# Kernel optimization log

Hardware: AMD Instinct MI355X
Metric: run time of the kernel (lower is better)

The kernel has to match this reference:

```python
import jax, jax.numpy as jnp
import numpy as np

NUM_EMBEDDINGS = 768
HEAD_SIZE = 64

def setup_inputs() -> dict:
    key = jax.random.key(0)
    kx, kq, kk, kv = jax.random.split(key, 4)
    B, T, E, H = 4, 2048, NUM_EMBEDDINGS, HEAD_SIZE
    x = jax.random.normal(kx, (B, T, E), dtype=jnp.float32)
    s = 1.0 / np.sqrt(E)
    Wq = jax.random.normal(kq, (E, H), dtype=jnp.float32) * s
    Wk = jax.random.normal(kk, (E, H), dtype=jnp.float32) * s
    Wv = jax.random.normal(kv, (E, H), dtype=jnp.float32) * s
    return {"x": x, "Wq": Wq, "Wk": Wk, "Wv": Wv}

def reference(x, Wq, Wk, Wv):
    # x: [B,T,E]; Wq/Wk/Wv: [E,H]
    q = x @ Wq  # [B,T,H]
    k = x @ Wk
    v = x @ Wv
    scores = jnp.einsum('bth,bsh->bts', q, k) * (k.shape[-1] ** -0.5)  # [B,T,T]
    T = scores.shape[-1]
    # torch.tril(ones, diagonal=-1).bool(): True strictly below diagonal (t > s)
    row = jnp.arange(T)[:, None]
    col = jnp.arange(T)[None, :]
    mask = row > col  # strictly lower triangle masked to -inf
    scores = jnp.where(mask, -jnp.inf, scores)
    attn = jax.nn.softmax(scores, axis=-1)
    return attn @ v  # [B,T,H]
```

## Files before the change

### kernel.cpp

```cpp
#include <hip/hip_runtime.h>
#include <hip/hip_bf16.h>

#define T_ 2048
#define E_ 768

typedef __attribute__((ext_vector_type(8))) __bf16 bf16x8;
typedef __attribute__((ext_vector_type(8))) unsigned short ushort8;
typedef __attribute__((ext_vector_type(4))) unsigned short ushort4v;
typedef __attribute__((ext_vector_type(4))) float floatx4;

static __device__ __forceinline__ unsigned short f2bf(float f) {
    union { float f; unsigned u; } v; v.f = f;
    unsigned u = v.u;
    u += 0x7FFFu + ((u >> 16) & 1u);
    return (unsigned short)(u >> 16);
}

static __device__ __forceinline__ float bf2f(unsigned short s) {
    union { unsigned u; float f; } v; v.u = ((unsigned)s) << 16;
    return v.f;
}

__global__ __launch_bounds__(256) void prep_wT(const float* __restrict__ Wq,
                                               const float* __restrict__ Wk,
                                               const float* __restrict__ Wv,
                                               unsigned short* __restrict__ wT) {
    int w  = blockIdx.x / 12;
    int k0 = (blockIdx.x % 12) * 64;
    const float* W = (w == 0) ? Wq : (w == 1 ? Wk : Wv);
    __shared__ unsigned short sm[64][65];
    int tid = threadIdx.x;
    #pragma unroll
    for (int i = 0; i < 16; ++i) {
        int idx = tid + i * 256;
        int k = idx >> 6, n = idx & 63;
        sm[n][k] = f2bf(W[(size_t)(k0 + k) * 64 + n]);
    }
    __syncthreads();
    #pragma unroll
    for (int i = 0; i < 16; ++i) {
        int idx = tid + i * 256;
        int n = idx >> 6, k = idx & 63;
        wT[(size_t)w * (64 * 768) + (size_t)n * 768 + k0 + k] = sm[n][k];
    }
}

__global__ __launch_bounds__(256) void qkv_proj(const float* __restrict__ x,
                                                const unsigned short* __restrict__ wT,
                                                unsigned short* __restrict__ Qb,
                                                unsigned short* __restrict__ Kb,
                                                unsigned short* __restrict__ vT) {
    __shared__ unsigned short ws_[192][72];
    __shared__ unsigned short xs[16][72];

    int tid  = threadIdx.x;
    int lane = tid & 63, wv = tid >> 6;
    int lrow = lane & 15;
    int kh   = lane >> 4;
    int lk   = kh * 8;
    int t0   = blockIdx.x * 16;
    int n0   = wv * 48;

    int wr = tid >> 3;
    int wc = (tid & 7) * 8;
    int xr = tid >> 4;
    int xc = (tid & 15) * 4;

    floatx4 acc[3] = {};

    for (int k0 = 0; k0 < 768; k0 += 64) {
        #pragma unroll
        for (int c = 0; c < 6; ++c) {
            int rw = c * 32 + wr;
            *(ushort8*)&ws_[rw][wc] = *(const ushort8*)(wT + (size_t)rw * 768 + k0 + wc);
        }
        {
            float4 a = *(const float4*)(x + (size_t)(t0 + xr) * 768 + k0 + xc);
            ushort4v p;
            p[0] = f2bf(a.x); p[1] = f2bf(a.y); p[2] = f2bf(a.z); p[3] = f2bf(a.w);
            *(ushort4v*)&xs[xr][xc] = p;
        }
        __syncthreads();
        #pragma unroll
        for (int kc = 0; kc < 2; ++kc) {
            bf16x8 af = *(const bf16x8*)&xs[lrow][kc * 32 + lk];
            #pragma unroll
            for (int nf = 0; nf < 3; ++nf) {
                bf16x8 bfv = *(const bf16x8*)&ws_[n0 + nf * 16 + lrow][kc * 32 + lk];
                acc[nf] = __builtin_amdgcn_mfma_f32_16x16x32_bf16(af, bfv, acc[nf], 0, 0, 0);
            }
        }
        __syncthreads();
    }

    const float QS = 0.18033688011112042f;
    int mt = t0 + kh * 4;
    #pragma unroll
    for (int nf = 0; nf < 3; ++nf) {
        int nb   = n0 + nf * 16;
        int widx = nb >> 6;
        int col  = (nb & 63) + lrow;
        if (widx == 0) {
            #pragma unroll
            for (int rg = 0; rg < 4; ++rg)
                Qb[(size_t)(mt + rg) * 64 + col] = f2bf(acc[nf][rg] * QS);
        } else if (widx == 1) {
            #pragma unroll
            for (int rg = 0; rg < 4; ++rg)
                Kb[(size_t)(mt + rg) * 64 + col] = f2bf(acc[nf][rg]);
        } else {
            int b  = mt >> 11;
            int tl = mt & 2047;
            ushort4v pk;
            #pragma unroll
            for (int rg = 0; rg < 4; ++rg) pk[rg] = f2bf(acc[nf][rg]);
            *(ushort4v*)&vT[(size_t)(b * 64 + col) * T_ + tl] = pk;
        }
    }
}

__global__ __launch_bounds__(256) void attn_one(const unsigned short* __restrict__ Qb,
                                                const unsigned short* __restrict__ Kb,
                                                const unsigned short* __restrict__ vT,
                                                float* __restrict__ lP,
                                                unsigned short* __restrict__ oP) {
    int c  = blockIdx.x;
    int qt = blockIdx.y;
    int b  = blockIdx.z;
    int t0 = qt * 64;
    int s0 = t0 + c * 64;
    if (s0 >= T_) return;

    __shared__ unsigned short ks[64][72];
    __shared__ unsigned short vts[64][72];
    __shared__ unsigned short ps[4][16][72];

    int tid  = threadIdx.x;
    int lane = tid & 63, wv = tid >> 6;
    int lrow = lane & 15;
    int lk   = (lane >> 4) * 8;
    int qrow4 = (lane >> 4) * 4;
    int sr = tid >> 2, sc = tid & 3;

    const ushort8* kp = (const ushort8*)(Kb + (size_t)(b * T_ + s0 + sr) * 64 + sc * 16);
    ushort8 ka = kp[0], kb = kp[1];
    const ushort8* vp = (const ushort8*)(vT + (size_t)(b * 64 + sr) * T_ + s0 + sc * 16);
    ushort8 va = vp[0], vb = vp[1];
    bf16x8 qf[2];
    {
        const unsigned short* qp = Qb + (size_t)(b * T_ + t0 + wv * 16 + lrow) * 64 + lk;
        qf[0] = *(const bf16x8*)(qp);
        qf[1] = *(const bf16x8*)(qp + 32);
    }
    *(ushort8*)&ks[sr][sc * 16]      = ka;
    *(ushort8*)&ks[sr][sc * 16 + 8]  = kb;
    *(ushort8*)&vts[sr][sc * 16]     = va;
    *(ushort8*)&vts[sr][sc * 16 + 8] = vb;
    __syncthreads();

    floatx4 sf[4] = {};
    #pragma unroll
    for (int kc = 0; kc < 2; ++kc) {
        bf16x8 af = qf[kc];
        #pragma unroll
        for (int nf = 0; nf < 4; ++nf) {
            bf16x8 bfv = *(const bf16x8*)&ks[nf * 16 + lrow][kc * 32 + lk];
            sf[nf] = __builtin_amdgcn_mfma_f32_16x16x32_bf16(af, bfv, sf[nf], 0, 0, 0);
        }
    }

    if (c == 0) {
        #pragma unroll
        for (int nf = 0; nf < 4; ++nf)
            #pragma unroll
            for (int rg = 0; rg < 4; ++rg) {
                int sl = nf * 16 + lrow;
                int ql = wv * 16 + qrow4 + rg;
                if (sl < ql) sf[nf][rg] = -__builtin_inff();
            }
    }

    float l_[4] = {0.f, 0.f, 0.f, 0.f};
    #pragma unroll
    for (int nf = 0; nf < 4; ++nf)
        #pragma unroll
        for (int rg = 0; rg < 4; ++rg) {
            float p = exp2f(sf[nf][rg]);
            l_[rg] += p;
            ps[wv][qrow4 + rg][nf * 16 + lrow] = f2bf(p);
        }

    floatx4 of[4] = {};
    #pragma unroll
    for (int kc = 0; kc < 2; ++kc) {
        bf16x8 pa = *(const bf16x8*)&ps[wv][lrow][kc * 32 + lk];
        #pragma unroll
        for (int hf = 0; hf < 4; ++hf) {
            bf16x8 vbv = *(const bf16x8*)&vts[hf * 16 + lrow][kc * 32 + lk];
            of[hf] = __builtin_amdgcn_mfma_f32_16x16x32_bf16(pa, vbv, of[hf], 0, 0, 0);
        }
    }

    int p = ((b * 32 + qt) << 5) + c;
    #pragma unroll
    for (int rg = 0; rg < 4; ++rg) {
        float v = l_[rg];
        v += __shfl_xor(v, 1, 64);
        v += __shfl_xor(v, 2, 64);
        v += __shfl_xor(v, 4, 64);
        v += __shfl_xor(v, 8, 64);
        l_[rg] = v;
    }
    if (lrow == 0) {
        #pragma unroll
        for (int rg = 0; rg < 4; ++rg) {
            int row = wv * 16 + qrow4 + rg;
            lP[(size_t)p * 64 + row] = l_[rg];
        }
    }
    #pragma unroll
    for (int hf = 0; hf < 4; ++hf)
        #pragma unroll
        for (int rg = 0; rg < 4; ++rg) {
            int row = wv * 16 + qrow4 + rg;
            oP[((size_t)p * 64 + row) * 64 + hf * 16 + lrow] = f2bf(of[hf][rg]);
        }
}

__global__ __launch_bounds__(256) void combine(const float* __restrict__ lP,
                                               const unsigned short* __restrict__ oP,
                                               float* __restrict__ out) {
    int bq = blockIdx.x >> 2;
    int rq = blockIdx.x & 3;
    int qt = bq & 31;
    int b  = bq >> 5;
    int nch = 32 - qt;

    int tid = threadIdx.x;
    int r   = rq * 16 + (tid >> 4);
    int cb  = (tid & 15) * 4;

    float L = 0.f;
    float4 o = {0.f, 0.f, 0.f, 0.f};
    for (int cc = 0; cc < nch; ++cc) {
        size_t p = (size_t)((bq << 5) + cc);
        L += lP[p * 64 + r];
        ushort4v ov = *(const ushort4v*)&oP[(p * 64 + r) * 64 + cb];
        o.x += bf2f(ov[0]); o.y += bf2f(ov[1]); o.z += bf2f(ov[2]); o.w += bf2f(ov[3]);
    }
    float inv = 1.0f / L;
    float4 res = {o.x * inv, o.y * inv, o.z * inv, o.w * inv};
    *(float4*)&out[((size_t)(b * T_ + qt * 64 + r)) * 64 + cb] = res;
}

extern "C" void kernel_launch(void* const* d_in, const int* in_sizes, int n_in,
                              void* d_out, int out_size, void* d_ws, size_t ws_size,
                              hipStream_t stream) {
    const float* x  = (const float*)d_in[0];
    const float* Wq = (const float*)d_in[1];
    const float* Wk = (const float*)d_in[2];
    const float* Wv = (const float*)d_in[3];
    float* out = (float*)d_out;

    unsigned short* wT = (unsigned short*)d_ws;
    unsigned short* Qb = wT + 3 * 64 * 768;
    unsigned short* Kb = Qb + 8192 * 64;
    unsigned short* vT = Kb + 8192 * 64;
    float* lP = (float*)(vT + 4 * 64 * T_);
    unsigned short* oP = (unsigned short*)(lP + 128 * 32 * 64);

    prep_wT<<<36, 256, 0, stream>>>(Wq, Wk, Wv, wT);
    qkv_proj<<<512, 256, 0, stream>>>(x, wT, Qb, Kb, vT);
    attn_one<<<dim3(32, 32, 4), 256, 0, stream>>>(Qb, Kb, vT, lP, oP);
    combine<<<512, 256, 0, stream>>>(lP, oP, out);
}
```

Baseline: 48.65 us.

## Process four key tiles per attention block with direct-to-LDS swizzled loads

Each attention block now covers up to four 64-key tiles instead of one and accumulates l and O across them, so there are fewer partials for the combine pass to read and fewer blocks to launch. K, V^T and the weight tiles are stored pre-swizzled in global memory and copied straight into unpadded LDS with global_load_lds, with XOR-swizzled reads to avoid bank conflicts. The cost is less parallelism per block, serial work inside each block, and a layout coupling between the producer and consumer kernels.

New measurement: 41.84 us. 1.16x faster.

```diff
diff --git a/kernel.cpp b/kernel.cpp
--- a/kernel.cpp
+++ b/kernel.cpp
@@ -19,6 +19,12 @@
 static __device__ __forceinline__ float bf2f(unsigned short s) {
     union { unsigned u; float f; } v; v.u = ((unsigned)s) << 16;
     return v.f;
+}
+
+static __device__ __forceinline__ void gload16(const void* g, void* l) {
+    __builtin_amdgcn_global_load_lds(
+        (const __attribute__((address_space(1))) void*)g,
+        (__attribute__((address_space(3))) void*)l, 16, 0, 0);
 }
 
 __global__ __launch_bounds__(256) void prep_wT(const float* __restrict__ Wq,
@@ -41,7 +47,9 @@
     for (int i = 0; i < 16; ++i) {
         int idx = tid + i * 256;
         int n = idx >> 6, k = idx & 63;
-        wT[(size_t)w * (64 * 768) + (size_t)n * 768 + k0 + k] = sm[n][k];
+        int ng = w * 64 + n;
+        int swzk = ((((k >> 3) & 7) ^ (ng & 7)) << 3) | (k & 7);
+        wT[(size_t)w * (64 * 768) + (size_t)n * 768 + k0 + swzk] = sm[n][k];
     }
 }
 
@@ -50,7 +58,7 @@
                                                 unsigned short* __restrict__ Qb,
                                                 unsigned short* __restrict__ Kb,
                                                 unsigned short* __restrict__ vT) {
-    __shared__ unsigned short ws_[192][72];
+    __shared__ unsigned short ws_[192][64];
     __shared__ unsigned short xs[16][72];
 
     int tid  = threadIdx.x;
@@ -61,18 +69,20 @@
     int t0   = blockIdx.x * 16;
     int n0   = wv * 48;
 
-    int wr = tid >> 3;
-    int wc = (tid & 7) * 8;
     int xr = tid >> 4;
     int xc = (tid & 15) * 4;
 
+    int wrow_l = (lane >> 3);
+    int wslot  = lane & 7;
+
     floatx4 acc[3] = {};
 
     for (int k0 = 0; k0 < 768; k0 += 64) {
         #pragma unroll
         for (int c = 0; c < 6; ++c) {
-            int rw = c * 32 + wr;
-            *(ushort8*)&ws_[rw][wc] = *(const ushort8*)(wT + (size_t)rw * 768 + k0 + wc);
+            int rbase = wv * 48 + c * 8;
+            const unsigned short* src = wT + (size_t)(rbase + wrow_l) * 768 + k0 + wslot * 8;
+            gload16(src, &ws_[rbase][0]);
         }
         {
             float4 a = *(const float4*)(x + (size_t)(t0 + xr) * 768 + k0 + xc);
@@ -84,9 +94,10 @@
         #pragma unroll
         for (int kc = 0; kc < 2; ++kc) {
             bf16x8 af = *(const bf16x8*)&xs[lrow][kc * 32 + lk];
+            int sl = (kc * 4 + kh) ^ (lrow & 7);
             #pragma unroll
             for (int nf = 0; nf < 3; ++nf) {
-                bf16x8 bfv = *(const bf16x8*)&ws_[n0 + nf * 16 + lrow][kc * 32 + lk];
+                bf16x8 bfv = *(const bf16x8*)&ws_[n0 + nf * 16 + lrow][sl << 3];
                 acc[nf] = __builtin_amdgcn_mfma_f32_16x16x32_bf16(af, bfv, acc[nf], 0, 0, 0);
             }
         }
@@ -106,20 +117,26 @@
                 Qb[(size_t)(mt + rg) * 64 + col] = f2bf(acc[nf][rg] * QS);
         } else if (widx == 1) {
             #pragma unroll
-            for (int rg = 0; rg < 4; ++rg)
-                Kb[(size_t)(mt + rg) * 64 + col] = f2bf(acc[nf][rg]);
+            for (int rg = 0; rg < 4; ++rg) {
+                int krow = mt + rg;
+                int g    = col >> 3;
+                int c2   = (((g ^ (krow & 7)) << 3)) | (col & 7);
+                Kb[(size_t)krow * 64 + c2] = f2bf(acc[nf][rg]);
+            }
         } else {
             int b  = mt >> 11;
             int tl = mt & 2047;
+            int h  = col;
+            int tswz = (tl & ~63) | ((((tl >> 3) & 7) ^ (h & 7)) << 3) | (tl & 7);
             ushort4v pk;
             #pragma unroll
             for (int rg = 0; rg < 4; ++rg) pk[rg] = f2bf(acc[nf][rg]);
-            *(ushort4v*)&vT[(size_t)(b * 64 + col) * T_ + tl] = pk;
-        }
-    }
-}
-
-__global__ __launch_bounds__(256) void attn_one(const unsigned short* __restrict__ Qb,
+            *(ushort4v*)&vT[(size_t)(b * 64 + h) * T_ + tswz] = pk;
+        }
+    }
+}
+
+__global__ __launch_bounds__(256) void attn_sum(const unsigned short* __restrict__ Qb,
                                                 const unsigned short* __restrict__ Kb,
                                                 const unsigned short* __restrict__ vT,
                                                 float* __restrict__ lP,
@@ -128,80 +145,92 @@
     int qt = blockIdx.y;
     int b  = blockIdx.z;
     int t0 = qt * 64;
-    int s0 = t0 + c * 64;
-    if (s0 >= T_) return;
-
-    __shared__ unsigned short ks[64][72];
-    __shared__ unsigned short vts[64][72];
+    int sBeg = t0 + c * 256;
+    if (sBeg >= T_) return;
+    int nt = (T_ - sBeg) >> 6; if (nt > 4) nt = 4;
+
+    __shared__ unsigned short ks4[4][64][64];
+    __shared__ unsigned short vts4[4][64][64];
     __shared__ unsigned short ps[4][16][72];
 
     int tid  = threadIdx.x;
     int lane = tid & 63, wv = tid >> 6;
     int lrow = lane & 15;
-    int lk   = (lane >> 4) * 8;
-    int qrow4 = (lane >> 4) * 4;
-    int sr = tid >> 2, sc = tid & 3;
-
-    const ushort8* kp = (const ushort8*)(Kb + (size_t)(b * T_ + s0 + sr) * 64 + sc * 16);
-    ushort8 ka = kp[0], kb = kp[1];
-    const ushort8* vp = (const ushort8*)(vT + (size_t)(b * 64 + sr) * T_ + s0 + sc * 16);
-    ushort8 va = vp[0], vb = vp[1];
+    int kh   = lane >> 4;
+    int lk   = kh * 8;
+    int qrow4 = kh * 4;
+    int rsub = lane >> 3;
+    int gsub = lane & 7;
+
+    for (int i = 0; i < nt; ++i) {
+        int s0 = sBeg + i * 64;
+        const unsigned short* ksrc = Kb + (size_t)(b * T_ + s0 + wv * 16 + rsub) * 64 + gsub * 8;
+        gload16(ksrc,                 &ks4[i][wv * 16][0]);
+        gload16(ksrc + 8 * 64,        &ks4[i][wv * 16 + 8][0]);
+        const unsigned short* vsrc = vT + (size_t)(b * 64 + wv * 16 + rsub) * T_ + s0 + gsub * 8;
+        gload16(vsrc,                 &vts4[i][wv * 16][0]);
+        gload16(vsrc + 8 * (size_t)T_, &vts4[i][wv * 16 + 8][0]);
+    }
+
     bf16x8 qf[2];
     {
         const unsigned short* qp = Qb + (size_t)(b * T_ + t0 + wv * 16 + lrow) * 64 + lk;
         qf[0] = *(const bf16x8*)(qp);
         qf[1] = *(const bf16x8*)(qp + 32);
     }
-    *(ushort8*)&ks[sr][sc * 16]      = ka;
-    *(ushort8*)&ks[sr][sc * 16 + 8]  = kb;
-    *(ushort8*)&vts[sr][sc * 16]     = va;
-    *(ushort8*)&vts[sr][sc * 16 + 8] = vb;
+
     __syncthreads();
 
-    floatx4 sf[4] = {};
-    #pragma unroll
-    for (int kc = 0; kc < 2; ++kc) {
-        bf16x8 af = qf[kc];
-        #pragma unroll
-        for (int nf = 0; nf < 4; ++nf) {
-            bf16x8 bfv = *(const bf16x8*)&ks[nf * 16 + lrow][kc * 32 + lk];
-            sf[nf] = __builtin_amdgcn_mfma_f32_16x16x32_bf16(af, bfv, sf[nf], 0, 0, 0);
-        }
-    }
-
-    if (c == 0) {
+    float l_[4] = {0.f, 0.f, 0.f, 0.f};
+    floatx4 of[4] = {};
+
+    for (int i = 0; i < nt; ++i) {
+        bool domask = (c == 0) && (i == 0);
+        floatx4 sf[4] = {};
+        #pragma unroll
+        for (int kc = 0; kc < 2; ++kc) {
+            bf16x8 af = qf[kc];
+            int sl = (kc * 4 + kh) ^ (lrow & 7);
+            #pragma unroll
+            for (int nf = 0; nf < 4; ++nf) {
+                bf16x8 bfv = *(const bf16x8*)&ks4[i][nf * 16 + lrow][sl << 3];
+                sf[nf] = __builtin_amdgcn_mfma_f32_16x16x32_bf16(af, bfv, sf[nf], 0, 0, 0);
+            }
+        }
+
+        if (domask) {
+            #pragma unroll
+            for (int nf = 0; nf < 4; ++nf)
+                #pragma unroll
+                for (int rg = 0; rg < 4; ++rg) {
+                    int slane = nf * 16 + lrow;
+                    int qlane = wv * 16 + qrow4 + rg;
+                    if (slane < qlane) sf[nf][rg] = -__builtin_inff();
+                }
+        }
+
         #pragma unroll
         for (int nf = 0; nf < 4; ++nf)
             #pragma unroll
             for (int rg = 0; rg < 4; ++rg) {
-                int sl = nf * 16 + lrow;
-                int ql = wv * 16 + qrow4 + rg;
-                if (sl < ql) sf[nf][rg] = -__builtin_inff();
-            }
-    }
-
-    float l_[4] = {0.f, 0.f, 0.f, 0.f};
-    #pragma unroll
-    for (int nf = 0; nf < 4; ++nf)
-        #pragma unroll
-        for (int rg = 0; rg < 4; ++rg) {
-            float p = exp2f(sf[nf][rg]);
-            l_[rg] += p;
-            ps[wv][qrow4 + rg][nf * 16 + lrow] = f2bf(p);
-        }
-
-    floatx4 of[4] = {};
-    #pragma unroll
-    for (int kc = 0; kc < 2; ++kc) {
-        bf16x8 pa = *(const bf16x8*)&ps[wv][lrow][kc * 32 + lk];
-        #pragma unroll
-        for (int hf = 0; hf < 4; ++hf) {
-            bf16x8 vbv = *(const bf16x8*)&vts[hf * 16 + lrow][kc * 32 + lk];
-            of[hf] = __builtin_amdgcn_mfma_f32_16x16x32_bf16(pa, vbv, of[hf], 0, 0, 0);
-        }
-    }
-
-    int p = ((b * 32 + qt) << 5) + c;
+                float p = exp2f(sf[nf][rg]);
+                l_[rg] += p;
+                ps[wv][qrow4 + rg][nf * 16 + lrow] = f2bf(p);
+            }
+
+        #pragma unroll
+        for (int kc = 0; kc < 2; ++kc) {
+            bf16x8 pa = *(const bf16x8*)&ps[wv][lrow][kc * 32 + lk];
+            int sl = (kc * 4 + kh) ^ (lrow & 7);
+            #pragma unroll
+            for (int hf = 0; hf < 4; ++hf) {
+                bf16x8 vbv = *(const bf16x8*)&vts4[i][hf * 16 + lrow][sl << 3];
+                of[hf] = __builtin_amdgcn_mfma_f32_16x16x32_bf16(pa, vbv, of[hf], 0, 0, 0);
+            }
+        }
+    }
+
+    int p = (b * 32 + qt) * 8 + c;
     #pragma unroll
     for (int rg = 0; rg < 4; ++rg) {
         float v = l_[rg];
@@ -234,7 +263,7 @@
     int rq = blockIdx.x & 3;
     int qt = bq & 31;
     int b  = bq >> 5;
-    int nch = 32 - qt;
+    int nch = (2303 - 64 * qt) >> 8;
 
     int tid = threadIdx.x;
     int r   = rq * 16 + (tid >> 4);
@@ -243,7 +272,7 @@
     float L = 0.f;
     float4 o = {0.f, 0.f, 0.f, 0.f};
     for (int cc = 0; cc < nch; ++cc) {
-        size_t p = (size_t)((bq << 5) + cc);
+        size_t p = (size_t)(bq * 8 + cc);
         L += lP[p * 64 + r];
         ushort4v ov = *(const ushort4v*)&oP[(p * 64 + r) * 64 + cb];
         o.x += bf2f(ov[0]); o.y += bf2f(ov[1]); o.z += bf2f(ov[2]); o.w += bf2f(ov[3]);
@@ -267,10 +296,10 @@
     unsigned short* Kb = Qb + 8192 * 64;
     unsigned short* vT = Kb + 8192 * 64;
     float* lP = (float*)(vT + 4 * 64 * T_);
-    unsigned short* oP = (unsigned short*)(lP + 128 * 32 * 64);
+    unsigned short* oP = (unsigned short*)(lP + 128 * 8 * 64);
 
     prep_wT<<<36, 256, 0, stream>>>(Wq, Wk, Wv, wT);
     qkv_proj<<<512, 256, 0, stream>>>(x, wT, Qb, Kb, vT);
-    attn_one<<<dim3(32, 32, 4), 256, 0, stream>>>(Qb, Kb, vT, lP, oP);
+    attn_sum<<<dim3(8, 32, 4), 256, 0, stream>>>(Qb, Kb, vT, lP, oP);
     combine<<<512, 256, 0, stream>>>(lP, oP, out);
 }
```
